# Optimization experiments

Hardware: AMD Instinct MI355X
Metric: run time of the kernel (lower is better)

## Reference

```python
import jax, jax.numpy as jnp
import numpy as np

PS, R, FS, SS = 3, 2, 3, 10.0
PAD = (PS - 1) // 2  # 1


def extract_patches(x, ps, stride):
    # x: (C, Hp, Wp) already padded -> (C, ps, ps, ho, wo)
    C, Hp, Wp = x.shape
    ho = (Hp - ps) // stride + 1
    wo = (Wp - ps) // stride + 1
    rows = []
    for i in range(ps):
        cols = []
        for j in range(ps):
            cols.append(x[:, i:i + stride * ho:stride, j:j + stride * wo:stride])
        rows.append(jnp.stack(cols, axis=1))
    return jnp.stack(rows, axis=1)


def fuse_diag(S):
    # conv2d of (L,L) 'image' with eye(3) kernel, zero pad 1:
    # out[u,v] = S[u-1,v-1] + S[u,v] + S[u+1,v+1]
    Sp = jnp.pad(S, 1)
    return Sp[:-2, :-2] + Sp[1:-1, 1:-1] + Sp[2:, 2:]


def ca_single(f, b, mask):
    # f, b: (c, h, w); mask: (1, h, w)
    c, h, w = f.shape
    # full-res background patches (replicate pad, stride R) -> reconstruction bank
    b_pad = jnp.pad(b, ((0, 0), (PAD, PAD), (PAD, PAD)), mode='edge')
    bg = extract_patches(b_pad, PS, R)                 # (c,ps,ps,hr,wr)
    hr, wr = bg.shape[3], bg.shape[4]
    L = hr * wr
    bg = bg.reshape(c, PS, PS, L).transpose(3, 0, 1, 2)  # (L,c,ps,ps)
    # nearest 1/R downsample (F.interpolate nearest == strided pick)
    fl = f[:, ::R, ::R]
    bl = b[:, ::R, ::R]
    ml = mask[:, ::R, ::R]
    # shrunk background patches (replicate pad, stride 1) -> matching bank
    bl_pad = jnp.pad(bl, ((0, 0), (PAD, PAD), (PAD, PAD)), mode='edge')
    bgs = extract_patches(bl_pad, PS, 1).reshape(c, PS, PS, L).transpose(3, 0, 1, 2)
    # mask patches (zero pad), valid iff patch mean == 0
    mp = extract_patches(jnp.pad(ml, ((0, 0), (PAD, PAD), (PAD, PAD))), PS, 1)
    mi = (mp.mean(axis=(1, 2)).reshape(L) == 0.0).astype(f.dtype)  # (L,)
    # L2-normalize matching patches (clamped at 1e-4)
    bnorm = jnp.maximum(jnp.sqrt((bgs ** 2).sum(axis=(1, 2, 3))), 1e-4)
    bgs_n = bgs / bnorm[:, None, None, None]
    # score = conv2d(f, patches) with zero pad 1 -> cosine-like correlation
    fp = extract_patches(jnp.pad(fl, ((0, 0), (PAD, PAD), (PAD, PAD))), PS, 1)
    score = jnp.einsum('cijhw,lcij->lhw', fp, bgs_n)   # (L,hr,wr)
    # two-pass diagonal 'fuse' trick
    S = fuse_diag(score.reshape(L, L))
    S = S.reshape(hr, wr, hr, wr).transpose(1, 0, 3, 2).reshape(L, L)
    S = fuse_diag(S)
    score = S.reshape(wr, hr, wr, hr).transpose(1, 0, 3, 2).reshape(L, hr, wr)
    # masked softmax over the L patch axis
    score = score * mi[:, None, None]
    score = jax.nn.softmax(score * SS, axis=0) * mi[:, None, None]
    # conv_transpose2d(score, bg, stride=R, padding=PAD) / 4
    # == conv of R-dilated score with flipped kernel, pad = PS-1-PAD
    w_flip = bg[:, :, ::-1, ::-1].transpose(1, 0, 2, 3)  # (c,L,ps,ps)
    out = jax.lax.conv_general_dilated(
        score[None], w_flip, window_strides=(1, 1),
        padding=[(PS - 1 - PAD, PS - 1 - PAD)] * 2, lhs_dilation=(R, R),
        dimension_numbers=('NCHW', 'OIHW', 'NCHW'))[0] / 4.0  # (c,2hr-1,2wr-1)
    if out.shape[1] % 2 == 1:  # static shape check, matches torch branch
        out = jnp.pad(out, ((0, 0), (0, 1), (0, 1)), mode='edge')
    return out


def setup_inputs() -> dict:
    key = jax.random.key(0)
    k1, k2, k3 = jax.random.split(key, 3)
    B, c, h, w = 4, 128, 128, 128
    f = jax.random.normal(k1, (B, c, h, w), dtype=jnp.float32)
    b = jax.random.normal(k2, (B, c, h, w), dtype=jnp.float32)
    mask = jax.random.bernoulli(k3, 0.25, (B, 1, h, w)).astype(jnp.float32)
    return {'f': f, 'b': b, 'mask': mask}


def reference(f, b, mask):
    return jax.vmap(ca_single)(f, b, mask)
```

## Files before the change

### kernel.cpp

```cpp
#include <hip/hip_runtime.h>
#include <cstdint>

#define LVAL 4096
#define K1 1152
#define NT1 18
#define CCH 128
#define HH 128
#define WW 128
#define SSCALE 10.0f
#define NUPAD 2048
#define NACTPAD 512
#define PADPIX 4356
#define PIMG 557568

typedef __attribute__((ext_vector_type(8))) short short8;
typedef __attribute__((ext_vector_type(8))) _Float16 half8;
typedef __attribute__((ext_vector_type(4))) float f32x4;

static __device__ __forceinline__ int clampi(int v, int lo, int hi) {
    return v < lo ? lo : (v > hi ? hi : v);
}
static __device__ __forceinline__ unsigned short f2h(float x) {
    union { _Float16 h; unsigned short u; } c; c.h = (_Float16)x; return c.u;
}
static __device__ __forceinline__ float h2f(unsigned short u) {
    union { _Float16 h; unsigned short u; } c; c.u = u; return (float)c.h;
}

__global__ __launch_bounds__(256) void dst_kernel(const float* __restrict__ f,
        const float* __restrict__ b, unsigned short* __restrict__ fpad4,
        unsigned short* __restrict__ bpad4) {
    __shared__ float t[32][65];
    int h = blockIdx.x;
    int cg = blockIdx.y;
    int za = blockIdx.z;
    int img = za >> 1, arr = za & 1;
    const float* src = (arr ? b : f) + (size_t)img * CCH * HH * WW;
    unsigned short* dst = (arr ? bpad4 : fpad4) + (size_t)img * PIMG;
    int tid = threadIdx.x;
    int w = tid & 63, csub = tid >> 6;
    #pragma unroll
    for (int cc = 0; cc < 8; ++cc) {
        int cl = csub * 8 + cc;
        int ch = cg * 32 + cl;
        t[cl][w] = src[(size_t)ch * (HH * WW) + (2 * h) * WW + (2 * w)];
    }
    __syncthreads();
    int c = tid & 31, pr = tid >> 5;
    #pragma unroll
    for (int pp = 0; pp < 8; ++pp) {
        int w2 = pr * 8 + pp;
        dst[((size_t)(h + 1) * 66 + (w2 + 1)) * 128 + cg * 32 + c] = f2h(t[c][w2]);
    }
}

__global__ __launch_bounds__(256) void qk_border_kernel(unsigned short* __restrict__ fpad4,
        unsigned short* __restrict__ bpad4, float* __restrict__ Q) {
    int img = blockIdx.y;
    int tid = threadIdx.x;
    if (blockIdx.x < 1024) {
        int lane = tid & 63, sub = tid >> 6;
        int pix = blockIdx.x * 4 + sub;
        const unsigned short* row = bpad4 + (size_t)img * PIMG
                                    + ((size_t)((pix >> 6) + 1) * 66 + (pix & 63) + 1) * 128;
        uint32_t hv = *(const uint32_t*)(row + lane * 2);
        float a = h2f((unsigned short)(hv & 0xffff));
        float b2 = h2f((unsigned short)(hv >> 16));
        float s = a * a + b2 * b2;
        for (int off = 32; off > 0; off >>= 1) s += __shfl_xor(s, off, 64);
        if (lane == 0) Q[img * 4096 + pix] = s;
    } else {
        int id = (blockIdx.x - 1024) * 256 + tid;
        if (id >= PADPIX * 16) return;
        int pix = id >> 4, cg = (id & 15) << 3;
        int hp = pix / 66, wp = pix - hp * 66;
        if (hp >= 1 && hp <= 64 && wp >= 1 && wp <= 64) return;
        unsigned short* fp = fpad4 + (size_t)img * PIMG + (size_t)pix * 128 + cg;
        #pragma unroll
        for (int cc = 0; cc < 8; ++cc) fp[cc] = 0;
        int hs = clampi(hp - 1, 0, 63), wsx = clampi(wp - 1, 0, 63);
        const unsigned short* sb = bpad4 + (size_t)img * PIMG
                                   + ((size_t)(hs + 1) * 66 + (wsx + 1)) * 128 + cg;
        unsigned short* bp = bpad4 + (size_t)img * PIMG + (size_t)pix * 128 + cg;
        #pragma unroll
        for (int cc = 0; cc < 8; ++cc) bp[cc] = sb[cc];
    }
}

__global__ __launch_bounds__(1024) void compact_kernel(const float* __restrict__ mask,
        const float* __restrict__ Q, int* __restrict__ act, int* __restrict__ ulist,
        short* __restrict__ tapu, float* __restrict__ invn, int* __restrict__ hdr) {
    int img = blockIdx.x;
    const float* mk = mask + (size_t)img * HH * WW;
    const float* Qi = Q + img * 4096;
    int* acti = act + img * NACTPAD;
    int* uli = ulist + img * NUPAD;
    short* tpi = tapu + (size_t)img * NACTPAD * 12;
    float* invi = invn + (size_t)img * NUPAD;
    int* hd = hdr + img * 4;
    int tid = threadIdx.x;
    int lane = tid & 63, wv = tid >> 6;
    __shared__ unsigned char flag[4096];
    __shared__ short umap[4096];
    __shared__ int actl[NACTPAD];
    __shared__ float ssl[4096];
    __shared__ int wsum[16], woff[16];
    __shared__ int tot;

    int loc[4];
    int cnt = 0;
    #pragma unroll
    for (int k = 0; k < 4; ++k) {
        int a = tid * 4 + k;
        int hb = a >> 6, wb = a & 63;
        float s = 0.f;
        for (int di = -1; di <= 1; ++di)
            for (int dj = -1; dj <= 1; ++dj) {
                int hh = hb + di, w2 = wb + dj;
                if (hh >= 0 && hh < 64 && w2 >= 0 && w2 < 64)
                    s += mk[(2 * hh) * WW + 2 * w2];
            }
        loc[k] = (s == 0.f) ? 1 : 0;
        cnt += loc[k];
    }
    int pre = cnt;
    for (int off = 1; off < 64; off <<= 1) { int v = __shfl_up(pre, off, 64); if (lane >= off) pre += v; }
    if (lane == 63) wsum[wv] = pre;
    __syncthreads();
    if (tid == 0) { int a2 = 0; for (int w2 = 0; w2 < 16; ++w2) { woff[w2] = a2; a2 += wsum[w2]; } tot = a2; }
    __syncthreads();
    int base = woff[wv] + pre - cnt;
    int n_act = tot < NACTPAD ? tot : NACTPAD;
    {
        int p = base;
        #pragma unroll
        for (int k = 0; k < 4; ++k)
            if (loc[k]) { if (p < NACTPAD) { acti[p] = tid * 4 + k; actl[p] = tid * 4 + k; } p++; }
    }
    #pragma unroll
    for (int k = 0; k < 4; ++k) { flag[tid * 4 + k] = 0; umap[tid * 4 + k] = -1; }
    __syncthreads();
    for (int j = tid; j < n_act; j += 1024) {
        int a = actl[j];
        int sa = ((a & 63) << 6) + (a >> 6);
        #pragma unroll
        for (int ei = 0; ei < 3; ++ei) {
            int tbt = sa + ei - 1;
            if (tbt < 0 || tbt >= 4096) continue;
            int tb = ((tbt & 63) << 6) + (tbt >> 6);
            #pragma unroll
            for (int d = -1; d <= 1; ++d) {
                int rb = tb + d;
                if (rb >= 0 && rb < 4096) flag[rb] = 1;
            }
        }
    }
    __syncthreads();
    int cnt2 = 0;
    int loc2[4];
    #pragma unroll
    for (int k = 0; k < 4; ++k) { loc2[k] = flag[tid * 4 + k]; cnt2 += loc2[k]; }
    int pre2 = cnt2;
    for (int off = 1; off < 64; off <<= 1) { int v = __shfl_up(pre2, off, 64); if (lane >= off) pre2 += v; }
    if (lane == 63) wsum[wv] = pre2;
    __syncthreads();
    if (tid == 0) { int a2 = 0; for (int w2 = 0; w2 < 16; ++w2) { woff[w2] = a2; a2 += wsum[w2]; } tot = a2; }
    __syncthreads();
    int base2 = woff[wv] + pre2 - cnt2;
    int n_u = tot < NUPAD ? tot : NUPAD;
    {
        int p = base2;
        #pragma unroll
        for (int k = 0; k < 4; ++k)
            if (loc2[k]) { int ci = tid * 4 + k; if (p < NUPAD) { uli[p] = ci; umap[ci] = (short)p; } p++; }
    }
    __syncthreads();
    for (int j = tid; j < n_act; j += 1024) {
        int a = actl[j];
        int sa = ((a & 63) << 6) + (a >> 6);
        #pragma unroll
        for (int ei = 0; ei < 3; ++ei) {
            int tbt = sa + ei - 1;
            int ok = (tbt >= 0 && tbt < 4096);
            int tb = ok ? ((tbt & 63) << 6) + (tbt >> 6) : 0;
            #pragma unroll
            for (int d = -1; d <= 1; ++d) {
                short v = -1;
                if (ok) { int rb = tb + d; if (rb >= 0 && rb < 4096) v = umap[rb]; }
                tpi[j * 12 + ei * 3 + d + 1] = v;
            }
        }
    }
    for (int a = tid; a < 4096; a += 1024) {
        int hb = a >> 6, wb = a & 63;
        float s = 0.f;
        #pragma unroll
        for (int i = 0; i < 3; ++i)
            #pragma unroll
            for (int j2 = 0; j2 < 3; ++j2) {
                int hl = clampi(hb + i - 1, 0, 63);
                int wl = clampi(wb + j2 - 1, 0, 63);
                s += Qi[hl * 64 + wl];
            }
        ssl[a] = s;
    }
    for (int u = tid; u < NUPAD; u += 1024) invi[u] = 0.f;
    __syncthreads();
    for (int ci = tid; ci < 4096; ci += 1024) {
        if (flag[ci]) {
            int u = umap[ci];
            if (u >= 0) invi[u] = 1.f / fmaxf(sqrtf(ssl[ci]), 1e-4f);
        }
    }
    if (tid == 0) { hd[0] = n_act; hd[1] = n_u; }
}

__global__ void prep_bgtc_kernel(const float* __restrict__ b, const int* __restrict__ act,
                                 const int* __restrict__ hdr, unsigned short* __restrict__ BGTc4) {
    int gimg = blockIdx.y;
    const float* bi = b + (size_t)gimg * CCH * HH * WW;
    int idx = blockIdx.x * 256 + threadIdx.x;
    int k2 = idx >> 9, j = idx & 511;
    int n_act = hdr[gimg * 4];
    unsigned short v = 0;
    if (j < n_act) {
        int a = act[gimg * NACTPAD + j];
        int ch = k2 & 127, q = k2 >> 7;
        int i = q / 3, jj = q - i * 3;
        int y = clampi(2 * (a >> 6) + i - 1, 0, 127);
        int x = clampi(2 * (a & 63) + jj - 1, 0, 127);
        v = f2h(bi[(size_t)ch * (HH * WW) + y * WW + x]);
    }
    BGTc4[(size_t)gimg * K1 * NACTPAD + idx] = v;
}

#define BAR() __builtin_amdgcn_s_barrier()
#define WAITV6() asm volatile("s_waitcnt vmcnt(6)" ::: "memory")
#define WAITV0() asm volatile("s_waitcnt vmcnt(0)" ::: "memory")

#define STAGEX(tt, h) do {                                                              \
    int t_ = (tt);                                                                      \
    if (t_ < NT1) {                                                                     \
        const int isB_ = ((h) == 1 || (h) == 2);                                        \
        const int hi_ = ((h) >= 2) ? 1 : 0;                                             \
        int q_ = t_ >> 1;                                                               \
        int qi_ = (q_ * 11) >> 5;                                                       \
        int qj_ = q_ - qi_ * 3;                                                         \
        int toff_ = ((qi_ * 66 + qj_) << 7) + ((t_ & 1) << 6);                          \
        _Pragma("unroll")                                                               \
        for (int r_ = 0; r_ < 2; ++r_) {                                                \
            int sl_ = hi_ * 2 + r_;                                                     \
            const unsigned short* g_ = (isB_ ? bR[sl_] : aR[sl_]) + toff_;              \
            unsigned short* l_ = lds + (isB_ ? 32768 : 0) + ((t_ & 1) << 14)            \
                                 + ((hi_ * 128 + r_ * 64 + swb) << 6);                  \
            __builtin_amdgcn_global_load_lds((const uint32_t*)(const void*)g_,          \
                                             (uint32_t*)(void*)l_, 16, 0, 0);           \
        }                                                                               \
    } } while (0)

#define LDA4(dst, cur, ah) do {                                                         \
    _Pragma("unroll")                                                                   \
    for (int f_ = 0; f_ < 4; ++f_)                                                      \
    { _Pragma("unroll")                                                                 \
      for (int s_ = 0; s_ < 2; ++s_) {                                                  \
        int row_ = wm * 128 + ((ah) * 4 + f_) * 16 + row16;                             \
        int cs_ = ((s_ << 2) + kgrp) ^ (row16 & 7);                                     \
        dst[f_ * 2 + s_] = *(const half8*)(lds + ((cur) << 14) + (row_ << 6) + (cs_ << 3)); \
    } } } while (0)

#define LDB2(cur, bh) do {                                                              \
    _Pragma("unroll")                                                                   \
    for (int f_ = 0; f_ < 2; ++f_)                                                      \
    { _Pragma("unroll")                                                                 \
      for (int s_ = 0; s_ < 2; ++s_) {                                                  \
        int row_ = wn * 64 + ((bh) * 2 + f_) * 16 + row16;                              \
        int cs_ = ((s_ << 2) + kgrp) ^ (row16 & 7);                                     \
        bv[(bh) * 4 + f_ * 2 + s_] = *(const half8*)(lds + 32768 + ((cur) << 14) + (row_ << 6) + (cs_ << 3)); \
    } } } while (0)

#define MFMA16(va, ai, bj) do {                                                         \
    __builtin_amdgcn_s_setprio(1);                                                      \
    _Pragma("unroll")                                                                   \
    for (int f_ = 0; f_ < 4; ++f_)                                                      \
    { _Pragma("unroll")                                                                 \
      for (int g_ = 0; g_ < 2; ++g_)                                                    \
      { _Pragma("unroll")                                                               \
        for (int s_ = 0; s_ < 2; ++s_)                                                  \
            acc[(ai) * 4 + f_][(bj) * 2 + g_] = __builtin_amdgcn_mfma_f32_16x16x32_f16( \
                va[f_ * 2 + s_], bv[(bj) * 4 + g_ * 2 + s_], acc[(ai) * 4 + f_][(bj) * 2 + g_], 0, 0, 0); \
    } } __builtin_amdgcn_s_setprio(0); } while (0)

__global__ __launch_bounds__(512, 2) void gemm1_8phase(const unsigned short* __restrict__ fpad4,
        const unsigned short* __restrict__ bpad4, unsigned short* __restrict__ Scc4,
        const int* __restrict__ ulist, const int* __restrict__ hdr,
        const float* __restrict__ invn) {
    __shared__ unsigned short lds[65536];
    const int gimg = blockIdx.y;
    const unsigned short* fpadI = fpad4 + (size_t)gimg * PIMG;
    const unsigned short* bpadI = bpad4 + (size_t)gimg * PIMG;
    unsigned short* C = Scc4 + (size_t)gimg * 4096 * NUPAD;
    const int* uli = ulist + gimg * NUPAD;
    const float* invi = invn + (size_t)gimg * NUPAD;
    const int n_u = hdr[gimg * 4 + 1];
    const int tid = threadIdx.x;
    const int lane = tid & 63;
    const int wave = tid >> 6;
    const int wm = wave >> 2, wn = wave & 3;
    const int row16 = lane & 15, kgrp = lane >> 4;
    const int srow = tid >> 3, schunk = tid & 7;
    const int swb = wave << 3;
    int bid = blockIdx.x;
    int wgid = ((bid & 7) << 4) + (bid >> 3);
    const int bm = (wgid >> 3) << 8;
    const int bn = (wgid & 7) << 8;
    if (bn >= ((n_u + 255) & ~255)) return;

    const int ck8 = (schunk ^ (srow & 7)) << 3;
    const unsigned short* aR[4];
    const unsigned short* bR[4];
    #pragma unroll
    for (int i2 = 0; i2 < 4; ++i2) {
        int rowp = i2 * 64 + srow;
        int ar = bm + rowp;
        aR[i2] = fpadI + (size_t)((ar >> 6) * 66 + (ar & 63)) * 128 + ck8;
        int uu = bn + rowp;
        int brow = uli[uu < n_u ? uu : n_u - 1];
        bR[i2] = bpadI + (size_t)((brow >> 6) * 66 + (brow & 63)) * 128 + ck8;
    }

    f32x4 acc[8][4];
    #pragma unroll
    for (int i = 0; i < 8; ++i)
        #pragma unroll
        for (int j = 0; j < 4; ++j)
            acc[i][j] = (f32x4){0.f, 0.f, 0.f, 0.f};

    STAGEX(0, 1); STAGEX(0, 2); STAGEX(0, 0); STAGEX(0, 3);
    STAGEX(1, 1); STAGEX(1, 2); STAGEX(1, 0);
    WAITV6();
    BAR();

    half8 av0[8], av1[8], bv[8];
    for (int t = 0; t < NT1; ++t) {
        const int cur = t & 1;
        LDA4(av0, cur, 0);
        LDB2(cur, 0);
        LDB2(cur, 1);
        STAGEX(t + 1, 3);
        BAR();
        MFMA16(av0, 0, 0);
        LDA4(av1, cur, 1);
        BAR();
        STAGEX(t + 2, 1);
        BAR();
        MFMA16(av0, 0, 1);
        BAR();
        STAGEX(t + 2, 2);
        BAR();
        MFMA16(av1, 1, 0);
        BAR();
        STAGEX(t + 2, 0);
        BAR();
        MFMA16(av1, 1, 1);
        if (t >= NT1 - 2) { WAITV0(); } else { WAITV6(); }
        BAR();
    }

    float iv[4];
    #pragma unroll
    for (int fj = 0; fj < 4; ++fj)
        iv[fj] = invi[bn + wn * 64 + fj * 16 + row16];
    #pragma unroll
    for (int fi = 0; fi < 8; ++fi) {
        int crow = bm + wm * 128 + fi * 16 + kgrp * 4;
        #pragma unroll
        for (int fj = 0; fj < 4; ++fj) {
            int ccol = bn + wn * 64 + fj * 16 + row16;
            f32x4 v = acc[fi][fj];
            #pragma unroll
            for (int r = 0; r < 4; ++r)
                C[(size_t)(crow + r) * NUPAD + ccol] = f2h(v[r] * iv[fj]);
        }
    }
}

__global__ __launch_bounds__(512) void fuse_softmax_kernel(const unsigned short* __restrict__ Scc4,
        const int* __restrict__ hdr, const short* __restrict__ tapu,
        unsigned short* __restrict__ Pc4) {
    __shared__ unsigned short lrow[3][NUPAD];
    __shared__ float redm[8][4], reds[8][4];
    int gimg = blockIdx.y;
    const unsigned short* Scc = Scc4 + (size_t)gimg * 4096 * NUPAD;
    int bid = blockIdx.x;
    int sb0 = ((bid & 7) << 9) + ((bid >> 3) << 2);
    int tid = threadIdx.x;
    int lane = tid & 63, wv = tid >> 6;
    int n_act = hdr[gimg * 4];
    int n_u = hdr[gimg * 4 + 1];
    int nu_s = (n_u + 15) & ~15;
    if (nu_s > NUPAD) nu_s = NUPAD;
    bool actv = tid < n_act;
    short tp[9];
    if (actv) {
        const short* tpp = tapu + ((size_t)gimg * NACTPAD + tid) * 12;
        #pragma unroll
        for (int t = 0; t < 9; ++t) tp[t] = tpp[t];
    }
    float s[4] = {0.f, 0.f, 0.f, 0.f};
    for (int ph = 0; ph < 6; ++ph) {
        int tt = sb0 - 1 + ph;
        int ok = (tt >= 0 && tt < 4096);
        int ta = ok ? ((tt & 63) << 6) + (tt >> 6) : 0;
        int vmask = 0;
        #pragma unroll
        for (int dp = 0; dp < 3; ++dp) {
            int ra = ta + dp - 1;
            if (ok && ra >= 0 && ra < 4096) {
                vmask |= 1 << dp;
                const unsigned short* src = Scc + (size_t)ra * NUPAD;
                for (int u = tid * 8; u < nu_s; u += 4096)
                    *(uint4*)&lrow[dp][u] = *(const uint4*)(src + u);
            }
        }
        __syncthreads();
        if (actv) {
            #pragma unroll
            for (int j = 0; j < 4; ++j) {
                int ei = ph - j;
                if (ei >= 0 && ei < 3) {
                    #pragma unroll
                    for (int dp = 0; dp < 3; ++dp) {
                        if ((vmask >> dp) & 1) {
                            int u = tp[ei * 3 + dp];
                            if (u >= 0) s[j] += h2f(lrow[dp][u]);
                        }
                    }
                }
            }
        }
        __syncthreads();
    }
    float m[4], e[4];
    #pragma unroll
    for (int j = 0; j < 4; ++j) {
        float x = actv ? SSCALE * s[j] : -3.0e38f;
        for (int off = 32; off > 0; off >>= 1) x = fmaxf(x, __shfl_xor(x, off, 64));
        if (lane == 0) redm[wv][j] = x;
    }
    __syncthreads();
    #pragma unroll
    for (int j = 0; j < 4; ++j) {
        float mm = -3.0e38f;
        #pragma unroll
        for (int w2 = 0; w2 < 8; ++w2) mm = fmaxf(mm, redm[w2][j]);
        m[j] = fmaxf(mm, 0.f);
        e[j] = actv ? __expf(SSCALE * s[j] - m[j]) : 0.f;
        float sm = e[j];
        for (int off = 32; off > 0; off >>= 1) sm += __shfl_xor(sm, off, 64);
        if (lane == 0) reds[wv][j] = sm;
    }
    __syncthreads();
    #pragma unroll
    for (int j = 0; j < 4; ++j) {
        float S = 0.f;
        #pragma unroll
        for (int w2 = 0; w2 < 8; ++w2) S += reds[w2][j];
        float denom = S + (4096.f - (float)n_act) * __expf(-m[j]);
        int sbj = sb0 + j;
        int b = ((sbj & 63) << 6) + (sbj >> 6);
        Pc4[(size_t)gimg * 4096 * NACTPAD + (size_t)b * NACTPAD + tid] = f2h(actv ? e[j] / denom : 0.f);
    }
}

__global__ __launch_bounds__(256) void gemm2_nt(
        const unsigned short* __restrict__ BGTc4, const unsigned short* __restrict__ Pc4,
        const int* __restrict__ hdr, unsigned short* __restrict__ OUTT4) {
    __shared__ unsigned short lds[2 * 128 * 64];
    unsigned short* Asm = lds;
    unsigned short* Bsm = lds + 128 * 64;
    const int gimg = blockIdx.z;
    const unsigned short* A = BGTc4 + (size_t)gimg * K1 * NACTPAD;
    const unsigned short* B = Pc4 + (size_t)gimg * 4096 * NACTPAD;
    unsigned short* C = OUTT4 + (size_t)gimg * K1 * LVAL;
    int n_act = hdr[gimg * 4];
    int kend = (n_act + 63) & ~63;
    if (kend < 64) kend = 64;
    const int tid = threadIdx.x;
    const int wave = tid >> 6, lane = tid & 63;
    const int wm = wave >> 1, wn = wave & 1;
    const int bm = blockIdx.y << 7, bn = blockIdx.x << 7;
    const int rsub = lane >> 3, csub = lane & 7;
    const int gcol = (csub ^ rsub) << 3;
    const int row16 = lane & 15, kgrp = lane >> 4;
    const int sw = (row16 & 7) << 3;

    f32x4 acc[4][4];
    #pragma unroll
    for (int i = 0; i < 4; ++i)
        #pragma unroll
        for (int j = 0; j < 4; ++j)
            acc[i][j] = (f32x4){0.f, 0.f, 0.f, 0.f};

    for (int k0 = 0; k0 < kend; k0 += 64) {
        __syncthreads();
        #pragma unroll
        for (int r = 0; r < 4; ++r) {
            int row = (wave << 5) + (r << 3) + rsub;
            const unsigned short* ga = A + (size_t)(bm + row) * NACTPAD + k0 + gcol;
            unsigned short* la = Asm + (((wave << 5) + (r << 3)) << 6);
            __builtin_amdgcn_global_load_lds((const uint32_t*)(const void*)ga,
                                             (uint32_t*)(void*)la, 16, 0, 0);
            const unsigned short* gb = B + (size_t)(bn + row) * NACTPAD + k0 + gcol;
            unsigned short* lb = Bsm + (((wave << 5) + (r << 3)) << 6);
            __builtin_amdgcn_global_load_lds((const uint32_t*)(const void*)gb,
                                             (uint32_t*)(void*)lb, 16, 0, 0);
        }
        __syncthreads();
        #pragma unroll
        for (int s = 0; s < 2; ++s) {
            half8 af[4], bfr[4];
            #pragma unroll
            for (int fi = 0; fi < 4; ++fi) {
                int ar = (wm << 6) + (fi << 4) + row16;
                af[fi] = *(const half8*)(Asm + (ar << 6) + (((s << 5) + (kgrp << 3)) ^ sw));
            }
            #pragma unroll
            for (int fj = 0; fj < 4; ++fj) {
                int br = (wn << 6) + (fj << 4) + row16;
                bfr[fj] = *(const half8*)(Bsm + (br << 6) + (((s << 5) + (kgrp << 3)) ^ sw));
            }
            #pragma unroll
            for (int fi = 0; fi < 4; ++fi)
                #pragma unroll
                for (int fj = 0; fj < 4; ++fj)
                    acc[fi][fj] = __builtin_amdgcn_mfma_f32_16x16x32_f16(
                        af[fi], bfr[fj], acc[fi][fj], 0, 0, 0);
        }
        __syncthreads();
    }
    #pragma unroll
    for (int fi = 0; fi < 4; ++fi) {
        int crow = bm + (wm << 6) + (fi << 4) + (kgrp << 2);
        #pragma unroll
        for (int fj = 0; fj < 4; ++fj) {
            int ccol = bn + (wn << 6) + (fj << 4) + row16;
            f32x4 v = acc[fi][fj];
            #pragma unroll
            for (int r = 0; r < 4; ++r)
                C[(size_t)(crow + r) * LVAL + ccol] = f2h(v[r]);
        }
    }
}

__global__ void scatter_kernel(const unsigned short* __restrict__ OUTT4,
                               float* __restrict__ out) {
    int gimg = blockIdx.y;
    const unsigned short* OUTT = OUTT4 + (size_t)gimg * K1 * LVAL;
    float* oi = out + (size_t)gimg * CCH * HH * WW;
    int idx = blockIdx.x * 256 + threadIdx.x;
    int x = idx & 127;
    int y = (idx >> 7) & 127;
    int ch = idx >> 14;
    int yy = y < 127 ? y : 126;
    int xx = x < 127 ? x : 126;
    int hy[2], iy[2], ny;
    if (yy & 1) { hy[0] = (yy + 1) >> 1; iy[0] = 0; hy[1] = (yy - 1) >> 1; iy[1] = 2; ny = 2; }
    else        { hy[0] = yy >> 1;       iy[0] = 1; ny = 1; }
    int wx[2], jx[2], nx;
    if (xx & 1) { wx[0] = (xx + 1) >> 1; jx[0] = 0; wx[1] = (xx - 1) >> 1; jx[1] = 2; nx = 2; }
    else        { wx[0] = xx >> 1;       jx[0] = 1; nx = 1; }
    float s = 0.f;
    for (int u = 0; u < ny; ++u)
        for (int v = 0; v < nx; ++v) {
            int k2 = (iy[u] * 3 + jx[v]) * 128 + ch;
            s += h2f(OUTT[(size_t)k2 * LVAL + (hy[u] << 6) + wx[v]]);
        }
    oi[idx] = s * 0.25f;
}

extern "C" void kernel_launch(void* const* d_in, const int* in_sizes, int n_in,
                              void* d_out, int out_size, void* d_ws, size_t ws_size,
                              hipStream_t stream) {
    const float* f = (const float*)d_in[0];
    const float* b = (const float*)d_in[1];
    const float* mask = (const float*)d_in[2];
    float* out = (float*)d_out;
    char* ws = (char*)d_ws;

    const size_t oQ    = 0;
    const size_t oACT  = 65536;
    const size_t oUL   = 73728;
    const size_t oTAP  = 106496;
    const size_t oHDR  = 155648;
    const size_t oINVN = 156672;
    const size_t oBGTC = 189440;
    const size_t oPC   = 4908032;
    const size_t oFPAD = 21685248;
    const size_t oBPAD = 26145792;
    const size_t oSCC  = 30606336;

    float* Q   = (float*)(ws + oQ);
    int*   ACT = (int*)(ws + oACT);
    int*   UL  = (int*)(ws + oUL);
    short* TAP = (short*)(ws + oTAP);
    int*   HDR = (int*)(ws + oHDR);
    float* INVN = (float*)(ws + oINVN);
    unsigned short* BGTc4 = (unsigned short*)(ws + oBGTC);
    unsigned short* Pc4   = (unsigned short*)(ws + oPC);
    unsigned short* fpad4 = (unsigned short*)(ws + oFPAD);
    unsigned short* bpad4 = (unsigned short*)(ws + oBPAD);
    unsigned short* Scc4 = (unsigned short*)(ws + oSCC);
    unsigned short* OUTT4 = (unsigned short*)(ws + oSCC);

    dst_kernel<<<dim3(64, 4, 8), 256, 0, stream>>>(f, b, fpad4, bpad4);
    qk_border_kernel<<<dim3(1297, 4), 256, 0, stream>>>(fpad4, bpad4, Q);
    compact_kernel<<<4, 1024, 0, stream>>>(mask, Q, ACT, UL, TAP, INVN, HDR);
    prep_bgtc_kernel<<<dim3(2304, 4), 256, 0, stream>>>(b, ACT, HDR, BGTc4);

    gemm1_8phase<<<dim3(128, 4), 512, 0, stream>>>(fpad4, bpad4, Scc4, UL, HDR, INVN);
    fuse_softmax_kernel<<<dim3(1024, 4), 512, 0, stream>>>(Scc4, HDR, TAP, Pc4);

    gemm2_nt<<<dim3(32, 9, 4), 256, 0, stream>>>(BGTc4, Pc4, HDR, OUTT4);
    scatter_kernel<<<dim3(8192, 4), 256, 0, stream>>>(OUTT4, out);
    (void)in_sizes; (void)n_in; (void)out_size; (void)ws_size;
}
```

Baseline: 222.7 us.

## Double-buffer gemm2 LDS loads and widen fuse_softmax to eight columns per block

gemm2_nt now uses two LDS stages and issues the next k-tile's global-to-LDS loads before the MFMAs on the current tile. This is meant to overlap memory latency with compute. Separately, fuse_softmax_kernel handles 8 output columns per block instead of 4, using 10 row-load phases instead of 6 and half as many blocks. That cuts redundant reloads of neighbouring score rows, at the cost of more registers and less block-level parallelism. WAITV0 is used but its definition is not visible.

```diff
diff --git a/kernel.cpp b/kernel.cpp
--- a/kernel.cpp
+++ b/kernel.cpp
@@ -388,11 +388,11 @@
         const int* __restrict__ hdr, const short* __restrict__ tapu,
         unsigned short* __restrict__ Pc4) {
     __shared__ unsigned short lrow[3][NUPAD];
-    __shared__ float redm[8][4], reds[8][4];
+    __shared__ float redm[8][8], reds[8][8];
     int gimg = blockIdx.y;
     const unsigned short* Scc = Scc4 + (size_t)gimg * 4096 * NUPAD;
     int bid = blockIdx.x;
-    int sb0 = ((bid & 7) << 9) + ((bid >> 3) << 2);
+    int sb0 = ((bid & 7) << 9) + ((bid >> 3) << 3);
     int tid = threadIdx.x;
     int lane = tid & 63, wv = tid >> 6;
     int n_act = hdr[gimg * 4];
@@ -406,8 +406,8 @@
         #pragma unroll
         for (int t = 0; t < 9; ++t) tp[t] = tpp[t];
     }
-    float s[4] = {0.f, 0.f, 0.f, 0.f};
-    for (int ph = 0; ph < 6; ++ph) {
+    float s[8] = {0.f, 0.f, 0.f, 0.f, 0.f, 0.f, 0.f, 0.f};
+    for (int ph = 0; ph < 10; ++ph) {
         int tt = sb0 - 1 + ph;
         int ok = (tt >= 0 && tt < 4096);
         int ta = ok ? ((tt & 63) << 6) + (tt >> 6) : 0;
@@ -425,7 +425,7 @@
         __syncthreads();
         if (actv) {
             #pragma unroll
-            for (int j = 0; j < 4; ++j) {
+            for (int j = 0; j < 8; ++j) {
                 int ei = ph - j;
                 if (ei >= 0 && ei < 3) {
                     #pragma unroll
@@ -440,16 +440,16 @@
         }
         __syncthreads();
     }
-    float m[4], e[4];
-    #pragma unroll
-    for (int j = 0; j < 4; ++j) {
+    float m[8], e[8];
+    #pragma unroll
+    for (int j = 0; j < 8; ++j) {
         float x = actv ? SSCALE * s[j] : -3.0e38f;
         for (int off = 32; off > 0; off >>= 1) x = fmaxf(x, __shfl_xor(x, off, 64));
         if (lane == 0) redm[wv][j] = x;
     }
     __syncthreads();
     #pragma unroll
-    for (int j = 0; j < 4; ++j) {
+    for (int j = 0; j < 8; ++j) {
         float mm = -3.0e38f;
         #pragma unroll
         for (int w2 = 0; w2 < 8; ++w2) mm = fmaxf(mm, redm[w2][j]);
@@ -461,7 +461,7 @@
     }
     __syncthreads();
     #pragma unroll
-    for (int j = 0; j < 4; ++j) {
+    for (int j = 0; j < 8; ++j) {
         float S = 0.f;
         #pragma unroll
         for (int w2 = 0; w2 < 8; ++w2) S += reds[w2][j];
@@ -472,12 +472,24 @@
     }
 }
 
+#define G2STAGE(bs, kk) do {                                                            \
+    _Pragma("unroll")                                                                   \
+    for (int r_ = 0; r_ < 4; ++r_) {                                                    \
+        int row_ = (wave << 5) + (r_ << 3) + rsub;                                      \
+        const unsigned short* ga_ = A + (size_t)(bm + row_) * NACTPAD + (kk) + gcol;    \
+        unsigned short* la_ = lds + (bs) * 16384 + (((wave << 5) + (r_ << 3)) << 6);    \
+        __builtin_amdgcn_global_load_lds((const uint32_t*)(const void*)ga_,             \
+                                         (uint32_t*)(void*)la_, 16, 0, 0);              \
+        const unsigned short* gb_ = B + (size_t)(bn + row_) * NACTPAD + (kk) + gcol;    \
+        unsigned short* lb_ = lds + (bs) * 16384 + 8192 + (((wave << 5) + (r_ << 3)) << 6); \
+        __builtin_amdgcn_global_load_lds((const uint32_t*)(const void*)gb_,             \
+                                         (uint32_t*)(void*)lb_, 16, 0, 0);              \
+    } } while (0)
+
 __global__ __launch_bounds__(256) void gemm2_nt(
         const unsigned short* __restrict__ BGTc4, const unsigned short* __restrict__ Pc4,
         const int* __restrict__ hdr, unsigned short* __restrict__ OUTT4) {
-    __shared__ unsigned short lds[2 * 128 * 64];
-    unsigned short* Asm = lds;
-    unsigned short* Bsm = lds + 128 * 64;
+    __shared__ unsigned short lds[2 * 16384];
     const int gimg = blockIdx.z;
     const unsigned short* A = BGTc4 + (size_t)gimg * K1 * NACTPAD;
     const unsigned short* B = Pc4 + (size_t)gimg * 4096 * NACTPAD;
@@ -501,21 +513,15 @@
         for (int j = 0; j < 4; ++j)
             acc[i][j] = (f32x4){0.f, 0.f, 0.f, 0.f};
 
-    for (int k0 = 0; k0 < kend; k0 += 64) {
-        __syncthreads();
-        #pragma unroll
-        for (int r = 0; r < 4; ++r) {
-            int row = (wave << 5) + (r << 3) + rsub;
-            const unsigned short* ga = A + (size_t)(bm + row) * NACTPAD + k0 + gcol;
-            unsigned short* la = Asm + (((wave << 5) + (r << 3)) << 6);
-            __builtin_amdgcn_global_load_lds((const uint32_t*)(const void*)ga,
-                                             (uint32_t*)(void*)la, 16, 0, 0);
-            const unsigned short* gb = B + (size_t)(bn + row) * NACTPAD + k0 + gcol;
-            unsigned short* lb = Bsm + (((wave << 5) + (r << 3)) << 6);
-            __builtin_amdgcn_global_load_lds((const uint32_t*)(const void*)gb,
-                                             (uint32_t*)(void*)lb, 16, 0, 0);
-        }
-        __syncthreads();
+    G2STAGE(0, 0);
+    WAITV0();
+    __syncthreads();
+    int nt = kend >> 6;
+    for (int t = 0; t < nt; ++t) {
+        const int cs = t & 1;
+        if (t + 1 < nt) G2STAGE(cs ^ 1, (t + 1) << 6);
+        const unsigned short* Asm = lds + cs * 16384;
+        const unsigned short* Bsm = lds + cs * 16384 + 8192;
         #pragma unroll
         for (int s = 0; s < 2; ++s) {
             half8 af[4], bfr[4];
@@ -536,6 +542,7 @@
                     acc[fi][fj] = __builtin_amdgcn_mfma_f32_16x16x32_f16(
                         af[fi], bfr[fj], acc[fi][fj], 0, 0, 0);
         }
+        WAITV0();
         __syncthreads();
     }
     #pragma unroll
@@ -618,7 +625,7 @@
     prep_bgtc_kernel<<<dim3(2304, 4), 256, 0, stream>>>(b, ACT, HDR, BGTc4);
 
     gemm1_8phase<<<dim3(128, 4), 512, 0, stream>>>(fpad4, bpad4, Scc4, UL, HDR, INVN);
-    fuse_softmax_kernel<<<dim3(1024, 4), 512, 0, stream>>>(Scc4, HDR, TAP, Pc4);
+    fuse_softmax_kernel<<<dim3(512, 4), 512, 0, stream>>>(Scc4, HDR, TAP, Pc4);
 
     gemm2_nt<<<dim3(32, 9, 4), 256, 0, stream>>>(BGTc4, Pc4, HDR, OUTT4);
     scatter_kernel<<<dim3(8192, 4), 256, 0, stream>>>(OUTT4, out);
```

New measurement: 218.7 us (median of 2 runs). Within noise of the previous version (-1.8%).
